# Kernel tuning notes

Measured on AMD Instinct MI355X. Metric: run time of the kernel, lower is better.

Reference implementation:

```python
import jax, jax.numpy as jnp
import numpy as np

NUM_SYMBOLS = 5
NUM_SUBCARRIERS = 33


def _dft_matrix(n):
    # Unitary DFT matrix: F[j,k] = exp(-2i*pi*j*k/n) / sqrt(n)
    omega = np.exp(-2j * np.pi / n)
    j, k = np.meshgrid(np.arange(n), np.arange(n))
    return (np.power(omega, j * k) / np.sqrt(n)).astype(np.complex64)


def setup_inputs() -> dict:
    key = jax.random.key(0)
    k1, k2 = jax.random.split(key)
    shape = (4096, NUM_SYMBOLS, 4, 4, NUM_SUBCARRIERS)  # (N, S, TXH, TXW, W)
    x_real = jax.random.normal(k1, shape, dtype=jnp.float32)
    x_imag = jax.random.normal(k2, shape, dtype=jnp.float32)
    F_sym = _dft_matrix(NUM_SYMBOLS)
    F_sub = _dft_matrix(NUM_SUBCARRIERS)
    return {
        "x_real": x_real,
        "x_imag": x_imag,
        "F_sym_real": jnp.asarray(F_sym.real, dtype=jnp.float32),
        "F_sym_imag": jnp.asarray(F_sym.imag, dtype=jnp.float32),
        "F_sub_real": jnp.asarray(F_sub.real, dtype=jnp.float32),
        "F_sub_imag": jnp.asarray(F_sub.imag, dtype=jnp.float32),
    }


def reference(x_real, x_imag, F_sym_real, F_sym_imag, F_sub_real, F_sub_imag):
    N, S, TXH, TXW, W = x_real.shape
    x = jax.lax.complex(x_real, x_imag).reshape(N, S, TXH * TXW, W)
    x = jnp.transpose(x, (0, 2, 1, 3))  # (N, A, S, W), A = TXH*TXW

    F_sym = jax.lax.complex(F_sym_real, F_sym_imag)  # (S, S)
    F_sub = jax.lax.complex(F_sub_real, F_sub_imag)  # (W, W)

    # 2D DFT across symbols (left) and subcarriers (right)
    X = jnp.einsum("st,natw->nasw", F_sym, x)
    X = jnp.einsum("nasw,wv->nasv", X, F_sub)

    # magnitude-square (power spectrum)
    X_mag_sq = (X.real * X.real + X.imag * X.imag).astype(jnp.complex64)

    # inverse 2D DFT (conjugate transposes) -> autocorrelation
    X = jnp.einsum("st,natw->nasw", F_sym.conj().T, X_mag_sq)
    X = jnp.einsum("nasw,wv->nasv", X, F_sub.conj().T)

    X = jnp.transpose(X, (0, 2, 1, 3))  # (N, S, A, W)
    return X.reshape(N, S, TXH, TXW, W)
```

## Files before the change

### kernel.cpp

```cpp
#include <hip/hip_runtime.h>

#define NS 5
#define NW 33
#define NA 16
#define SW 165
#define BUFS 99
#define NFR 17
#define SFS (NFR*NW)
#define MPW 5
#define GM 20
#define TPM 11
#define CPT 3
#define THREADS 256

#define C0T 3
#define C0E (C0T*NW*MPW)
#define IT0 8
#define C1T 2
#define C1E (C1T*NW*MPW)
#define IT1 6

typedef float f2 __attribute__((ext_vector_type(2)));

__device__ __forceinline__ void cmac_re(f2& z, f2 u, f2 f) {
    asm("v_pk_fma_f32 %0, %1, %2, %0 op_sel:[0,0,0] op_sel_hi:[1,0,1]"
        : "+v"(z) : "v"(u), "v"(f));
}
__device__ __forceinline__ void cmac_im(f2& z, f2 d, f2 f) {
    asm("v_pk_fma_f32 %0, %1, %2, %0 op_sel:[1,1,0] op_sel_hi:[0,1,1] neg_lo:[1,0,0]"
        : "+v"(z) : "v"(d), "v"(f));
}
__device__ __forceinline__ void cmacr(f2& z, f2 f, f2 Pp) {
    asm("v_pk_fma_f32 %0, %1, %2, %0 op_sel:[0,0,0] op_sel_hi:[1,1,1] neg_hi:[1,0,0]"
        : "+v"(z) : "v"(f), "v"(Pp));
}
__device__ __forceinline__ void pkfma(f2& z, f2 a, f2 b) {
    asm("v_pk_fma_f32 %0, %1, %2, %0 op_sel:[0,0,0] op_sel_hi:[1,1,1]"
        : "+v"(z) : "v"(a), "v"(b));
}
__device__ __forceinline__ f2 pkadd(f2 a, f2 b) {
    f2 r; asm("v_pk_add_f32 %0, %1, %2" : "=v"(r) : "v"(a), "v"(b)); return r;
}
__device__ __forceinline__ f2 pksub(f2 a, f2 b) {
    f2 r; asm("v_pk_add_f32 %0, %1, %2 neg_lo:[0,1] neg_hi:[0,1]"
              : "=v"(r) : "v"(a), "v"(b)); return r;
}
__device__ __forceinline__ f2 pkaddsub(f2 a, f2 b) {
    f2 r; asm("v_pk_add_f32 %0, %1, %2 neg_hi:[0,1]"
              : "=v"(r) : "v"(a), "v"(b)); return r;
}
__device__ __forceinline__ f2 pkmul_re(f2 u, f2 f) {
    f2 r; asm("v_pk_mul_f32 %0, %1, %2 op_sel:[0,0] op_sel_hi:[1,0]"
              : "=v"(r) : "v"(u), "v"(f)); return r;
}
__device__ __forceinline__ f2 pkmul(f2 a, f2 b) {
    f2 r; asm("v_pk_mul_f32 %0, %1, %2" : "=v"(r) : "v"(a), "v"(b)); return r;
}

#define STAGE_LOAD(R, DS, NT, CE_, NIT, T0)                                \
    _Pragma("unroll")                                                      \
    for (int i = 0; i < NIT; ++i) {                                        \
        const int e = lane + i * 64;                                       \
        f2 v = (f2){0.f, 0.f};                                             \
        int da = 0;                                                        \
        if (e < (CE_)) {                                                   \
            const int gq = e / ((NT) * NW), rq = e - gq * ((NT) * NW);     \
            const int tq = rq / NW, wq = rq - tq * NW;                     \
            const int Mq = Mw + gq;                                        \
            da = gq * BUFS + wq * (NT) + tq;                               \
            if (Mq < NM) {                                                 \
                const int nq = Mq >> 4, aq = Mq & 15;                      \
                const int go = (nq * NS + (T0) + tq) * (NA * NW) + aq * NW + wq; \
                v = (f2){x_real[go], x_imag[go]};                          \
            }                                                              \
        }                                                                  \
        R[i] = v; DS[i] = da;                                              \
    }

#define STAGE_WRITE(R, DS, CE_, NIT)                                       \
    _Pragma("unroll")                                                      \
    for (int i = 0; i < NIT; ++i) {                                        \
        const int e = lane + i * 64;                                       \
        if (e < (CE_)) wbuf[DS[i]] = R[i];                                 \
    }

#define COMPUTE_CHUNK(NT, TBASE)                                           \
    if (act) {                                                             \
        const f2* bp = wbuf + gg * BUFS;                                   \
        {                                               \
            f2 fv[CPT];                                                    \
            _Pragma("unroll")                                              \
            for (int k = 0; k < CPT; ++k) fv[k] = sFsub[c0 + k];           \
            _Pragma("unroll")                                              \
            for (int t = 0; t < (NT); ++t) {                               \
                const f2 xc = bp[t];                                       \
                _Pragma("unroll")                                          \
                for (int k = 0; k < CPT; ++k)                              \
                    V[(TBASE) + t][k] = pkmul_re(xc, fv[k]);               \
            }                                                              \
        }                                                                  \
        _Pragma("unroll 4")                                                \
        for (int wp = 1; wp <= 16; ++wp) {                                 \
            const int wq = NW - wp;                                        \
            f2 xcA[NT], xcB[NT];                                           \
            _Pragma("unroll")                                              \
            for (int t = 0; t < (NT); ++t) xcA[t] = bp[wp * (NT) + t];     \
            _Pragma("unroll")                                              \
            for (int t = 0; t < (NT); ++t) xcB[t] = bp[wq * (NT) + t];     \
            f2 fv[CPT];                                                    \
            _Pragma("unroll")                                              \
            for (int k = 0; k < CPT; ++k) fv[k] = sFsub[wp * NW + c0 + k]; \
            _Pragma("unroll")                                              \
            for (int t = 0; t < (NT); ++t) {                               \
                const f2 u = pkadd(xcA[t], xcB[t]);                        \
                const f2 d = pksub(xcA[t], xcB[t]);                        \
                _Pragma("unroll")                                          \
                for (int k = 0; k < CPT; ++k) {                            \
                    cmac_re(V[(TBASE) + t][k], u, fv[k]);                  \
                    cmac_im(V[(TBASE) + t][k], d, fv[k]);                  \
                }                                                          \
            }                                                              \
        }                                                                  \
    }

__global__ __launch_bounds__(THREADS, 6) void autocorr_kernel(
    const float* __restrict__ x_real, const float* __restrict__ x_imag,
    const float* __restrict__ Fsym_re, const float* __restrict__ Fsym_im,
    const float* __restrict__ Fsub_re, const float* __restrict__ Fsub_im,
    float* __restrict__ out, int NM, int write_complex)
{
    __shared__ f2 sFsym[NS * NS];
    __shared__ f2 sFsub[SFS];
    __shared__ f2 buf[GM * BUFS];

    const int tid = threadIdx.x;
    const int wave = tid >> 6;
    const int lane = tid & 63;
    const int Mw = blockIdx.x * GM + wave * MPW;
    f2* const wbuf = &buf[wave * MPW * BUFS];

    for (int i = tid; i < SFS; i += THREADS)
        sFsub[i] = (f2){Fsub_re[i], Fsub_im[i]};
    if (tid < NS * NS) sFsym[tid] = (f2){Fsym_re[tid], Fsym_im[tid]};

    {
        f2 rr0[IT0]; int ds0[IT0];
        STAGE_LOAD(rr0, ds0, C0T, C0E, IT0, 0);
        STAGE_WRITE(rr0, ds0, C0E, IT0);
    }
    __syncthreads();

    const int g = lane / TPM;
    const int j = lane - g * TPM;
    const bool act = (lane < MPW * TPM);
    const int gg = act ? g : 0;
    const int M = Mw + gg;
    const int c0 = 3 * j;

    f2 V[NS][CPT];

    COMPUTE_CHUNK(C0T, 0);

    {
        f2 rr1[IT1]; int ds1[IT1];
        STAGE_LOAD(rr1, ds1, C1T, C1E, IT1, C0T);
        STAGE_WRITE(rr1, ds1, C1E, IT1);
    }
    asm volatile("s_waitcnt lgkmcnt(0)" ::: "memory");

    COMPUTE_CHUNK(C1T, C0T);

    f2 T2[3][CPT];
#pragma unroll
    for (int p = 0; p < 3; ++p)
#pragma unroll
        for (int k = 0; k < CPT; ++k) T2[p][k] = (f2){0.f, 0.f};
    if (act) {
#pragma unroll
        for (int k = 0; k < CPT; ++k) {
            f2 a = V[1][k], b = V[4][k];
            V[1][k] = pkadd(a, b); V[4][k] = pksub(a, b);
            a = V[2][k]; b = V[3][k];
            V[2][k] = pkadd(a, b); V[3][k] = pksub(a, b);
        }
#pragma unroll
        for (int s = 0; s < NS; ++s) {
            const f2 f0 = sFsym[s * NS + 0];
            const f2 f1 = sFsym[s * NS + 1];
            const f2 fc2 = sFsym[s * NS + 2];
            f2 X[CPT];
#pragma unroll
            for (int k = 0; k < CPT; ++k) {
                X[k] = pkmul_re(V[0][k], f0);
                cmac_re(X[k], V[1][k], f1); cmac_im(X[k], V[4][k], f1);
                cmac_re(X[k], V[2][k], fc2); cmac_im(X[k], V[3][k], fc2);
            }
#pragma unroll
            for (int k = 0; k < CPT; ++k) {
                const float Pv = X[k].x * X[k].x + X[k].y * X[k].y;
                const f2 Pp = (f2){Pv, Pv};
#pragma unroll
                for (int p = 0; p < 3; ++p)
                    cmacr(T2[p][k], sFsym[s * NS + p], Pp);
            }
        }
        f2* const wb = wbuf + gg * BUFS;
#pragma unroll
        for (int k = 0; k < CPT; ++k)
#pragma unroll
            for (int p = 0; p < 3; ++p)
                wb[(c0 + k) * 3 + p] = T2[p][k];
    }
    asm volatile("s_waitcnt lgkmcnt(0)" ::: "memory");

    if (act) {
        const f2* bp = wbuf + gg * BUFS;
        if (!write_complex) {
            f2 Ypk[3][CPT];
            {
                f2 fw[CPT];
#pragma unroll
                for (int k = 0; k < CPT; ++k) fw[k] = sFsub[c0 + k];
#pragma unroll
                for (int p = 0; p < 3; ++p) {
                    const f2 tc = bp[p];
#pragma unroll
                    for (int k = 0; k < CPT; ++k)
                        Ypk[p][k] = pkmul(tc, fw[k]);
                }
            }
#pragma unroll 4
            for (int vp = 1; vp <= 16; ++vp) {
                const int vq = NW - vp;
                f2 e2[3];
#pragma unroll
                for (int p = 0; p < 3; ++p) {
                    const f2 ta = bp[vp * 3 + p];
                    const f2 tb = bp[vq * 3 + p];
                    e2[p] = pkaddsub(ta, tb);
                }
                f2 fw[CPT];
#pragma unroll
                for (int k = 0; k < CPT; ++k)
                    fw[k] = sFsub[vp * NW + c0 + k];
#pragma unroll
                for (int p = 0; p < 3; ++p)
#pragma unroll
                    for (int k = 0; k < CPT; ++k)
                        pkfma(Ypk[p][k], e2[p], fw[k]);
            }
            if (M < NM) {
                const int n = M >> 4, a = M & 15;
                const int obase = ((n * NS) * NA + a) * NW;
#pragma unroll
                for (int p = 0; p < 3; ++p) {
                    const int pp = (NS - p) % NS;
#pragma unroll
                    for (int k = 0; k < CPT; ++k) {
                        const int q = c0 + k;
                        const int qq = (NW - q) % NW;
                        const float Yr = Ypk[p][k].x + Ypk[p][k].y;
                        out[obase + p * (NA * NW) + q] = Yr;
                        out[obase + pp * (NA * NW) + qq] = Yr;
                    }
                }
            }
        } else {
            f2 Y[3][CPT];
#pragma unroll
            for (int p = 0; p < 3; ++p)
#pragma unroll
                for (int k = 0; k < CPT; ++k) Y[p][k] = (f2){0.f, 0.f};
            for (int v = 0; v < NW; ++v) {
                const int row = (v <= 16) ? v : (NW - v);
                const float sgn = (v <= 16) ? 1.f : -1.f;
                f2 tc[3];
#pragma unroll
                for (int p = 0; p < 3; ++p) tc[p] = bp[v * 3 + p];
                f2 fw[CPT];
#pragma unroll
                for (int k = 0; k < CPT; ++k) {
                    f2 f = sFsub[row * NW + c0 + k];
                    f.y *= sgn;
                    fw[k] = f;
                }
#pragma unroll
                for (int p = 0; p < 3; ++p)
#pragma unroll
                    for (int k = 0; k < CPT; ++k) {
                        Y[p][k].x = fmaf(tc[p].x, fw[k].x, Y[p][k].x);
                        Y[p][k].x = fmaf(tc[p].y, fw[k].y, Y[p][k].x);
                        Y[p][k].y = fmaf(tc[p].y, fw[k].x, Y[p][k].y);
                        Y[p][k].y = fmaf(-tc[p].x, fw[k].y, Y[p][k].y);
                    }
            }
            if (M < NM) {
                const int n = M >> 4, a = M & 15;
#pragma unroll
                for (int p = 0; p < 3; ++p) {
                    const int pp = (NS - p) % NS;
#pragma unroll
                    for (int k = 0; k < CPT; ++k) {
                        const int q = c0 + k;
                        const int qq = (NW - q) % NW;
                        ((float2*)out)[((n * NS + p) * NA + a) * NW + q] =
                            make_float2(Y[p][k].x, Y[p][k].y);
                        ((float2*)out)[((n * NS + pp) * NA + a) * NW + qq] =
                            make_float2(Y[p][k].x, -Y[p][k].y);
                    }
                }
            }
        }
    }
}

extern "C" void kernel_launch(void* const* d_in, const int* in_sizes, int n_in,
                              void* d_out, int out_size, void* d_ws, size_t ws_size,
                              hipStream_t stream) {
    const float* x_real  = (const float*)d_in[0];
    const float* x_imag  = (const float*)d_in[1];
    const float* Fsym_re = (const float*)d_in[2];
    const float* Fsym_im = (const float*)d_in[3];
    const float* Fsub_re = (const float*)d_in[4];
    const float* Fsub_im = (const float*)d_in[5];

    const int NM = in_sizes[0] / SW;
    const long long n_cplx = (long long)in_sizes[0];
    const int write_complex = ((long long)out_size >= 2 * n_cplx) ? 1 : 0;

    const int blocks = (NM + GM - 1) / GM;

    autocorr_kernel<<<blocks, THREADS, 0, stream>>>(
        x_real, x_imag, Fsym_re, Fsym_im, Fsub_re, Fsub_im,
        (float*)d_out, NM, write_complex);
}
```

Measured before the change: 159.1 us.

## Factor 33-point subcarrier DFT into 3x11 Good-Thomas decomposition

Replaces the direct 33-point forward DFT in the first stage with a prime-factor (3x11) decomposition. An 11-point DFT with conjugate-pair symmetry is followed by a 3-point butterfly, and each thread's output columns change from contiguous 3j..3j+2 to a strided set {3j, 3j+11, 3j+22}. This is meant to cut the FMA count of the forward subcarrier transform. The occupancy hint drops from 6 to 5 waves to make room for the extra registers. The change relies on a specific Fsub row layout for its twiddles (row 3, index m) and on a hardcoded 1/sqrt(33) scale, which ties correctness to the unitary DFT input.

Measured after the change: 296.9 us. 86.6% more time.

```diff
diff --git a/kernel.cpp b/kernel.cpp
--- a/kernel.cpp
+++ b/kernel.cpp
@@ -22,6 +22,12 @@
 
 typedef float f2 __attribute__((ext_vector_type(2)));
 
+constexpr int W33[3][11] = {
+    { 0, 12, 24,  3, 15, 27,  6, 18, 30,  9, 21},
+    {22,  1, 13, 25,  4, 16, 28,  7, 19, 31, 10},
+    {11, 23,  2, 14, 26,  5, 17, 29,  8, 20, 32},
+};
+
 __device__ __forceinline__ void cmac_re(f2& z, f2 u, f2 f) {
     asm("v_pk_fma_f32 %0, %1, %2, %0 op_sel:[0,0,0] op_sel_hi:[1,0,1]"
         : "+v"(z) : "v"(u), "v"(f));
@@ -38,6 +44,10 @@
     asm("v_pk_fma_f32 %0, %1, %2, %0 op_sel:[0,0,0] op_sel_hi:[1,1,1]"
         : "+v"(z) : "v"(a), "v"(b));
 }
+__device__ __forceinline__ f2 pkfma3(f2 a, f2 b, f2 c) {
+    f2 r; asm("v_pk_fma_f32 %0, %1, %2, %3 op_sel:[0,0,0] op_sel_hi:[1,1,1]"
+              : "=v"(r) : "v"(a), "v"(b), "v"(c)); return r;
+}
 __device__ __forceinline__ f2 pkadd(f2 a, f2 b) {
     f2 r; asm("v_pk_add_f32 %0, %1, %2" : "=v"(r) : "v"(a), "v"(b)); return r;
 }
@@ -55,6 +65,10 @@
 }
 __device__ __forceinline__ f2 pkmul(f2 a, f2 b) {
     f2 r; asm("v_pk_mul_f32 %0, %1, %2" : "=v"(r) : "v"(a), "v"(b)); return r;
+}
+__device__ __forceinline__ f2 pkmul_i(f2 d, f2 ss) {
+    f2 r; asm("v_pk_mul_f32 %0, %1, %2 op_sel:[1,0] op_sel_hi:[0,1] neg_lo:[1,0]"
+              : "=v"(r) : "v"(d), "v"(ss)); return r;
 }
 
 #define STAGE_LOAD(R, DS, NT, CE_, NIT, T0)                                \
@@ -87,43 +101,44 @@
 #define COMPUTE_CHUNK(NT, TBASE)                                           \
     if (act) {                                                             \
         const f2* bp = wbuf + gg * BUFS;                                   \
-        {                                               \
-            f2 fv[CPT];                                                    \
+        f2 cb[5];                                                          \
+        {                                                                  \
+            int m_ = 0;                                                    \
             _Pragma("unroll")                                              \
-            for (int k = 0; k < CPT; ++k) fv[k] = sFsub[c0 + k];           \
-            _Pragma("unroll")                                              \
-            for (int t = 0; t < (NT); ++t) {                               \
-                const f2 xc = bp[t];                                       \
-                _Pragma("unroll")                                          \
-                for (int k = 0; k < CPT; ++k)                              \
-                    V[(TBASE) + t][k] = pkmul_re(xc, fv[k]);               \
+            for (int b = 1; b <= 5; ++b) {                                 \
+                m_ += j; if (m_ >= 11) m_ -= 11;                           \
+                cb[b - 1] = sFsub[3 * NW + m_];      \
             }                                                              \
         }                                                                  \
-        _Pragma("unroll 4")                                                \
-        for (int wp = 1; wp <= 16; ++wp) {                                 \
-            const int wq = NW - wp;                                        \
-            f2 xcA[NT], xcB[NT];                                           \
+        _Pragma("unroll")                                                  \
+        for (int t = 0; t < (NT); ++t) {                                   \
+            f2 Z[3];                                                       \
             _Pragma("unroll")                                              \
-            for (int t = 0; t < (NT); ++t) xcA[t] = bp[wp * (NT) + t];     \
-            _Pragma("unroll")                                              \
-            for (int t = 0; t < (NT); ++t) xcB[t] = bp[wq * (NT) + t];     \
-            f2 fv[CPT];                                                    \
-            _Pragma("unroll")                                              \
-            for (int k = 0; k < CPT; ++k) fv[k] = sFsub[wp * NW + c0 + k]; \
-            _Pragma("unroll")                                              \
-            for (int t = 0; t < (NT); ++t) {                               \
-                const f2 u = pkadd(xcA[t], xcB[t]);                        \
-                const f2 d = pksub(xcA[t], xcB[t]);                        \
+            for (int w3 = 0; w3 < 3; ++w3) {                               \
+                f2 acc = pkmul(bp[W33[w3][0] * (NT) + t], invs);           \
                 _Pragma("unroll")                                          \
-                for (int k = 0; k < CPT; ++k) {                            \
-                    cmac_re(V[(TBASE) + t][k], u, fv[k]);                  \
-                    cmac_im(V[(TBASE) + t][k], d, fv[k]);                  \
+                for (int b = 1; b <= 5; ++b) {                             \
+                    const f2 xa = bp[W33[w3][b] * (NT) + t];               \
+                    const f2 xb = bp[W33[w3][11 - b] * (NT) + t];          \
+                    const f2 u = pkadd(xa, xb);                            \
+                    const f2 d = pksub(xa, xb);                            \
+                    cmac_re(acc, u, cb[b - 1]);                            \
+                    cmac_im(acc, d, cb[b - 1]);                            \
                 }                                                          \
+                Z[w3] = acc;                                               \
             }                                                              \
+             \
+            const f2 u2 = pkadd(Z[1], Z[2]);                               \
+            const f2 d2 = pksub(Z[1], Z[2]);                               \
+            V[(TBASE) + t][0] = pkadd(Z[0], u2);                           \
+            const f2 zc = pkfma3(u2, cch, Z[0]);                           \
+            const f2 r2 = pkmul_i(d2, ssq);                                \
+            V[(TBASE) + t][1] = pkadd(zc, r2);                             \
+            V[(TBASE) + t][2] = pksub(zc, r2);                             \
         }                                                                  \
     }
 
-__global__ __launch_bounds__(THREADS, 6) void autocorr_kernel(
+__global__ __launch_bounds__(THREADS, 5) void autocorr_kernel(
     const float* __restrict__ x_real, const float* __restrict__ x_imag,
     const float* __restrict__ Fsym_re, const float* __restrict__ Fsym_im,
     const float* __restrict__ Fsub_re, const float* __restrict__ Fsub_im,
@@ -155,7 +170,20 @@
     const bool act = (lane < MPW * TPM);
     const int gg = act ? g : 0;
     const int M = Mw + gg;
-    const int c0 = 3 * j;
+
+    int Q[3];
+    {
+        const int q0 = 3 * j;
+        Q[0] = q0;
+        int q1 = q0 + 11; if (q1 >= 33) q1 -= 33;
+        int q2 = q0 + 22; if (q2 >= 33) q2 -= 33;
+        Q[1] = q1; Q[2] = q2;
+    }
+
+    const float INV33 = 0.17407765595569785f;
+    const f2 invs = (f2){INV33, INV33};
+    const f2 cch  = (f2){-0.5f, -0.5f};
+    const f2 ssq  = (f2){-0.8660254037844386f, -0.8660254037844386f};
 
     f2 V[NS][CPT];
 
@@ -209,7 +237,7 @@
         for (int k = 0; k < CPT; ++k)
 #pragma unroll
             for (int p = 0; p < 3; ++p)
-                wb[(c0 + k) * 3 + p] = T2[p][k];
+                wb[Q[k] * 3 + p] = T2[p][k];
     }
     asm volatile("s_waitcnt lgkmcnt(0)" ::: "memory");
 
@@ -220,7 +248,7 @@
             {
                 f2 fw[CPT];
 #pragma unroll
-                for (int k = 0; k < CPT; ++k) fw[k] = sFsub[c0 + k];
+                for (int k = 0; k < CPT; ++k) fw[k] = sFsub[Q[k]];
 #pragma unroll
                 for (int p = 0; p < 3; ++p) {
                     const f2 tc = bp[p];
@@ -242,7 +270,7 @@
                 f2 fw[CPT];
 #pragma unroll
                 for (int k = 0; k < CPT; ++k)
-                    fw[k] = sFsub[vp * NW + c0 + k];
+                    fw[k] = sFsub[vp * NW + Q[k]];
 #pragma unroll
                 for (int p = 0; p < 3; ++p)
 #pragma unroll
@@ -257,8 +285,8 @@
                     const int pp = (NS - p) % NS;
 #pragma unroll
                     for (int k = 0; k < CPT; ++k) {
-                        const int q = c0 + k;
-                        const int qq = (NW - q) % NW;
+                        const int q = Q[k];
+                        const int qq = (q == 0) ? 0 : (NW - q);
                         const float Yr = Ypk[p][k].x + Ypk[p][k].y;
                         out[obase + p * (NA * NW) + q] = Yr;
                         out[obase + pp * (NA * NW) + qq] = Yr;
@@ -280,7 +308,7 @@
                 f2 fw[CPT];
 #pragma unroll
                 for (int k = 0; k < CPT; ++k) {
-                    f2 f = sFsub[row * NW + c0 + k];
+                    f2 f = sFsub[row * NW + Q[k]];
                     f.y *= sgn;
                     fw[k] = f;
                 }
@@ -301,8 +329,8 @@
                     const int pp = (NS - p) % NS;
 #pragma unroll
                     for (int k = 0; k < CPT; ++k) {
-                        const int q = c0 + k;
-                        const int qq = (NW - q) % NW;
+                        const int q = Q[k];
+                        const int qq = (q == 0) ? 0 : (NW - q);
                         ((float2*)out)[((n * NS + p) * NA + a) * NW + q] =
                             make_float2(Y[p][k].x, Y[p][k].y);
                         ((float2*)out)[((n * NS + pp) * NA + a) * NW + qq] =
```
